# Kernel optimization log

Measured on AMD Instinct MI355X. Metric: run time of the kernel, lower is better.

The kernel has to match this reference:

```python
import jax, jax.numpy as jnp
import numpy as np
from math import sqrt

N_HEADS = 16

def setup_inputs() -> dict:
    key = jax.random.key(0)
    ks = jax.random.split(key, 6)
    B, T, C = 4, 2048, 1024
    s = 0.02
    return {
        "X": jax.random.normal(ks[0], (B, T, C), jnp.float32),
        "Wq": jax.random.normal(ks[1], (C, C), jnp.float32) * s,
        "Wk": jax.random.normal(ks[2], (C, C), jnp.float32) * s,
        "Wv": jax.random.normal(ks[3], (C, C), jnp.float32) * s,
        "Wo": jax.random.normal(ks[4], (C, C), jnp.float32) * s,
        "bo": jnp.zeros((C,), jnp.float32),
    }

def reference(X, Wq, Wk, Wv, Wo, bo):
    B, T, C = X.shape
    H = N_HEADS
    D = C // H
    scale = sqrt(C / H)  # == sqrt(D)
    # Linear layers (torch Linear: y = x @ W.T), split into heads: [B,H,T,D]
    Q = (X @ Wq.T).reshape(B, T, H, D).transpose(0, 2, 1, 3)
    K = (X @ Wk.T).reshape(B, T, H, D).transpose(0, 2, 1, 3)
    V = (X @ Wv.T).reshape(B, T, H, D).transpose(0, 2, 1, 3)
    A = jnp.einsum("bhtd,bhsd->bhts", Q, K) / scale  # [B,H,T,T]
    causal = jnp.tril(jnp.ones((T, T), dtype=bool))
    A = jnp.where(causal, A, -jnp.inf)
    A = jax.nn.softmax(A, axis=-1)
    Y = jnp.einsum("bhts,bhsd->bhtd", A, V)  # [B,H,T,D]
    Y = Y.transpose(0, 2, 1, 3).reshape(B, T, C)
    return Y @ Wo.T + bo
```

## Files before the change

### kernel.cpp

```cpp
#include <hip/hip_runtime.h>
#include <hip/hip_bf16.h>
#include <stdint.h>


typedef unsigned short u16;
typedef __attribute__((ext_vector_type(8))) __bf16 bf16x8;
typedef __attribute__((ext_vector_type(4))) float  f32x4;
typedef __attribute__((ext_vector_type(4))) unsigned short u16x4;
typedef __attribute__((ext_vector_type(8))) unsigned short u16x8;
typedef __attribute__((ext_vector_type(4))) short s16x4;

#define B_  4
#define T_  2048
#define C_  1024
#define H_  16
#define D_  64
#define BT_ (B_ * T_)
#define NT_ 16

#define Q_SCALE 0.1803368801111204f

__device__ __forceinline__ u16 f32_to_bf16(float f) {
    unsigned int u = __float_as_uint(f);
    unsigned int r = (u + 0x7FFFu + ((u >> 16) & 1u)) >> 16;
    return (u16)r;
}

__device__ __forceinline__ unsigned int pk_bf16(float a, float b) {
    float2 f2; f2.x = a; f2.y = b;
    __hip_bfloat162 h = __float22bfloat162_rn(f2);
    return *(unsigned int*)&h;
}

__device__ __forceinline__ void async16(const void* g, void* lds) {
    __builtin_amdgcn_global_load_lds(
        (const __attribute__((address_space(1))) void*)g,
        (__attribute__((address_space(3))) void*)lds, 16, 0, 0);
}

__global__ void cast_all_kernel(const float* __restrict__ X,
                                const float* __restrict__ w0, const float* __restrict__ w1,
                                const float* __restrict__ w2, const float* __restrict__ w3,
                                u16* __restrict__ xo,
                                u16* __restrict__ o0, u16* __restrict__ o1,
                                u16* __restrict__ o2, u16* __restrict__ o3) {
    int id = blockIdx.x;
    const float* in; u16* out; int i;
    if (id < 8192) {
        in = X; out = xo; i = id * 256 + threadIdx.x;
    } else {
        int k = (id - 8192) >> 10;
        in  = (k == 0) ? w0 : (k == 1) ? w1 : (k == 2) ? w2 : w3;
        out = (k == 0) ? o0 : (k == 1) ? o1 : (k == 2) ? o2 : o3;
        i = ((id - 8192) & 1023) * 256 + threadIdx.x;
    }
    float4 v = ((const float4*)in)[i];
    u16x4 o;
    o[0] = f32_to_bf16(v.x); o[1] = f32_to_bf16(v.y);
    o[2] = f32_to_bf16(v.z); o[3] = f32_to_bf16(v.w);
    ((u16x4*)out)[i] = o;
}

template<bool SWAP>
__device__ __forceinline__ void gemm8_core(const u16* __restrict__ Arow,
                                           const u16* __restrict__ Brow,
                                           char* lds, f32x4 (&acc)[4][4])
{
    int tid  = threadIdx.x;
    int lane = tid & 63, w = tid >> 6;
    int quad = lane >> 4, l15 = lane & 15;
    int wm = w >> 2, wn = w & 3;

    int r  = tid >> 2, s4 = tid & 3;
    int kg = ((s4 - (r >> 1)) & 3) * 8;
    const u16* xsrc  = Arow + (size_t)r * C_ + kg;
    const u16* wsrc0 = Brow + (size_t)r * C_ + kg;
    const u16* wsrc1 = Brow + (size_t)(128 + r) * C_ + kg;
    int wu = w << 10;

    int xoff[4], woff[4];
#pragma unroll
    for (int i = 0; i < 4; ++i) {
        int rx = wm * 64 + i * 16 + l15;
        xoff[i] = rx * 64 + (((rx >> 1) + quad) & 3) * 16;
        int rw = wn * 64 + i * 16 + l15;
        woff[i] = 16384 + rw * 64 + (((rw >> 1) + quad) & 3) * 16;
    }

    auto issue_group = [&](int g) {
        int db = (g >> 1) & 1, ks = g & 1;
        int koff = (g >> 1) * 64 + ks * 32;
        char* ldb = lds + db * 49152;
        async16(xsrc  + koff, ldb + ks * 8192 + wu);
        async16(wsrc0 + koff, ldb + 16384 + ks * 16384 + wu);
        async16(wsrc1 + koff, ldb + 16384 + ks * 16384 + 8192 + wu);
    };

    issue_group(0); issue_group(1); issue_group(2);
    asm volatile("s_waitcnt vmcnt(6)" ::: "memory");
    __builtin_amdgcn_s_barrier();
    asm volatile("" ::: "memory");

    for (int t = 0; t < NT_; ++t) {
        char* cb = lds + (t & 1) * 49152;
#pragma unroll
        for (int p = 0; p < 2; ++p) {
            bf16x8 xf[4], wf[4];
            const char* xb = cb + p * 8192;
            const char* wb = cb + p * 16384;
#pragma unroll
            for (int i = 0; i < 4; ++i) xf[i] = *(const bf16x8*)(xb + xoff[i]);
#pragma unroll
            for (int j = 0; j < 4; ++j) wf[j] = *(const bf16x8*)(wb + woff[j]);

            int g = 2 * t + 3 + p;
            if (g < 2 * NT_) issue_group(g);

            if (t < NT_ - 2) {
                asm volatile("s_waitcnt vmcnt(6)" ::: "memory");
            } else if (t == NT_ - 2) {
                if (p == 0) asm volatile("s_waitcnt vmcnt(6)" ::: "memory");
                else        asm volatile("s_waitcnt vmcnt(3)" ::: "memory");
            } else {
                if (p == 0) asm volatile("s_waitcnt vmcnt(0)" ::: "memory");
            }
            asm volatile("" ::: "memory");
            __builtin_amdgcn_s_barrier();
            asm volatile("" ::: "memory");

            __builtin_amdgcn_s_setprio(1);
#pragma unroll
            for (int i = 0; i < 4; ++i)
#pragma unroll
                for (int j = 0; j < 4; ++j) {
                    if (SWAP)
                        acc[i][j] = __builtin_amdgcn_mfma_f32_16x16x32_bf16(xf[i], wf[j], acc[i][j], 0, 0, 0);
                    else
                        acc[i][j] = __builtin_amdgcn_mfma_f32_16x16x32_bf16(wf[j], xf[i], acc[i][j], 0, 0, 0);
                }
            __builtin_amdgcn_s_setprio(0);
            asm volatile("" ::: "memory");
            __builtin_amdgcn_s_barrier();
            asm volatile("" ::: "memory");
        }
    }
}

__global__ __launch_bounds__(512, 2) void qkv_gemm8(
    const u16* __restrict__ Xb,
    const u16* __restrict__ Wqb, const u16* __restrict__ Wkb, const u16* __restrict__ Wvb,
    u16* __restrict__ Qb, u16* __restrict__ Kb, u16* __restrict__ Vtb)
{
    __shared__ __attribute__((aligned(128))) char LDSRAW[98304];

    int id = blockIdx.x;
    int wg = (id & 7) * 96 + (id >> 3);
    int bm = wg / 12, bn = wg % 12;
    int m0 = bm * 128;
    int nmat = bn >> 2;
    int chb  = (bn & 3) * 256;

    const u16* Wsel = (nmat == 0) ? Wqb : (nmat == 1) ? Wkb : Wvb;
    const u16* Arow = Xb   + (size_t)m0  * C_;
    const u16* Brow = Wsel + (size_t)chb * C_;

    f32x4 acc[4][4];
    const f32x4 z4 = {0.f, 0.f, 0.f, 0.f};
#pragma unroll
    for (int i = 0; i < 4; ++i)
#pragma unroll
        for (int j = 0; j < 4; ++j) acc[i][j] = z4;

    int tid = threadIdx.x, lane = tid & 63, w = tid >> 6;
    int quad = lane >> 4, l15 = lane & 15;
    int wm = w >> 2, wn = w & 3;

    if (nmat < 2) {
        gemm8_core<false>(Arow, Brow, LDSRAW, acc);
        u16* OUT = nmat ? Kb : Qb;
        float scale = nmat ? 1.0f : Q_SCALE;
#pragma unroll
        for (int i = 0; i < 4; ++i) {
            size_t trow = (size_t)(m0 + wm * 64 + i * 16 + l15) * C_;
#pragma unroll
            for (int j = 0; j < 4; ++j) {
                int ch = chb + wn * 64 + j * 16 + quad * 4;
                u16x4 v;
#pragma unroll
                for (int rr = 0; rr < 4; ++rr) v[rr] = f32_to_bf16(acc[i][j][rr] * scale);
                *(u16x4*)&OUT[trow + ch] = v;
            }
        }
    } else {
        gemm8_core<true>(Arow, Brow, LDSRAW, acc);
#pragma unroll
        for (int i = 0; i < 4; ++i) {
            int t0 = m0 + wm * 64 + i * 16 + quad * 4;
            int bb_ = t0 >> 11, tloc = t0 & (T_ - 1);
#pragma unroll
            for (int j = 0; j < 4; ++j) {
                int ch = chb + wn * 64 + j * 16 + l15;
                int h = ch >> 6, d = ch & 63;
                u16x4 v;
#pragma unroll
                for (int rr = 0; rr < 4; ++rr) v[rr] = f32_to_bf16(acc[i][j][rr]);
                *(u16x4*)&Vtb[(size_t)((bb_ * H_ + h) * D_ + d) * T_ + tloc] = v;
            }
        }
    }
}

__global__ __launch_bounds__(256, 4) void attn_kernel(
    const u16* __restrict__ Qb, const u16* __restrict__ Kb,
    const u16* __restrict__ Vtb, u16* __restrict__ Yb)
{
    __shared__ u16 SMA[16384];
    u16* Ks0 = SMA;
    u16* Ks1 = SMA + 4096;
    u16* Vs0 = SMA + 8192;
    u16* Vs1 = SMA + 12288;

    int id = blockIdx.x;
    int bh = id & 63;
    int jj = id >> 6;

    int tid = threadIdx.x, lane = tid & 63, w = tid >> 6;
    int quad = lane >> 4, l15 = lane & 15;
    int b = bh >> 4, h = bh & 15;

    int koff0[4], koff1[4], voff[4][4];
#pragma unroll
    for (int sblk = 0; sblk < 4; ++sblk) {
        int sr = sblk * 16 + l15;
        koff0[sblk] = (sr * 64 + ((quad + sr) & 7) * 8) * 2;
        koff1[sblk] = (sr * 64 + ((4 + quad + sr) & 7) * 8) * 2;
    }
#pragma unroll
    for (int n = 0; n < 4; ++n)
#pragma unroll
        for (int sblk = 0; sblk < 4; ++sblk) {
            int dr = n * 16 + l15;
            voff[n][sblk] = (dr * 64 + ((sblk * 2 + (quad >> 1) + dr) & 7) * 8 + (quad & 1) * 4) * 2;
        }

    int cA = tid, cB = tid + 256;
    int sA = cA >> 3, sB = cB >> 3;
    int offA = (((cA & 7) - sA) & 7) * 8;
    int offB = (((cB & 7) - sB) & 7) * 8;
    const u16* Kbase = Kb + (size_t)(b * T_) * C_ + h * 64;
    const u16* Vbase = Vtb + (size_t)bh * D_ * T_;
    int ldsb0 = (w * 64) * 16, ldsb1 = (256 + w * 64) * 16;

    const s16x4 ones = { (short)0x3F80, (short)0x3F80, (short)0x3F80, (short)0x3F80 };
    const f32x4 z4 = {0.f, 0.f, 0.f, 0.f};

    int qts[2] = { jj, 31 - jj };

    for (int pass = 0; pass < 2; ++pass) {
        int qt = qts[pass];
        int qbase = qt * 64;

        if (pass) __syncthreads();

        bf16x8 qf0, qf1;
        {
            const u16* q0 = Qb + ((size_t)(b * T_ + qbase + w * 16 + l15)) * C_ + h * 64;
            qf0 = *(const bf16x8*)(q0 + quad * 8);
            qf1 = *(const bf16x8*)(q0 + 32 + quad * 8);
        }

        f32x4 o_acc[4];
        f32x4 l_acc = z4;
#pragma unroll
        for (int n = 0; n < 4; ++n) o_acc[n] = z4;

        const int nst = qt + 1;

        const u16* kgpA = Kbase + (size_t)sA * C_ + offA;
        const u16* kgpB = Kbase + (size_t)sB * C_ + offB;
        const u16* vgpA = Vbase + sA * T_ + offA;
        const u16* vgpB = Vbase + sB * T_ + offB;

        async16(kgpA, (char*)Ks0 + ldsb0);
        async16(kgpB, (char*)Ks0 + ldsb1);
        async16(vgpA, (char*)Vs0 + ldsb0);
        async16(vgpB, (char*)Vs0 + ldsb1);
        kgpA += 64 * C_; kgpB += 64 * C_; vgpA += 64; vgpB += 64;

        auto tile_body = [&](int st, const u16* K_, const u16* V_, char* Kpf, char* Vpf) {
            __syncthreads();
            if (st + 1 < nst) {
                async16(kgpA, Kpf + ldsb0);
                async16(kgpB, Kpf + ldsb1);
                async16(vgpA, Vpf + ldsb0);
                async16(vgpB, Vpf + ldsb1);
            }
            kgpA += 64 * C_; kgpB += 64 * C_; vgpA += 64; vgpB += 64;

            f32x4 sv[4];
#pragma unroll
            for (int sblk = 0; sblk < 4; ++sblk) {
                bf16x8 k0 = *(const bf16x8*)((const char*)K_ + koff0[sblk]);
                bf16x8 k1 = *(const bf16x8*)((const char*)K_ + koff1[sblk]);
                f32x4 t0 = __builtin_amdgcn_mfma_f32_16x16x32_bf16(k0, qf0, z4, 0, 0, 0);
                sv[sblk] = __builtin_amdgcn_mfma_f32_16x16x32_bf16(k1, qf1, t0, 0, 0, 0);
            }

            if (st == qt) {
                int tl = w * 16 + l15;
#pragma unroll
                for (int sblk = 0; sblk < 4; ++sblk)
#pragma unroll
                    for (int r = 0; r < 4; ++r)
                        if (sblk * 16 + quad * 4 + r > tl) sv[sblk][r] = -1e30f;
            }

            s16x4 pfrag[4];
#pragma unroll
            for (int sblk = 0; sblk < 4; ++sblk) {
#pragma unroll
                for (int r = 0; r < 4; ++r)
                    sv[sblk][r] = __builtin_amdgcn_exp2f(sv[sblk][r]);
                uint2 pk;
                pk.x = pk_bf16(sv[sblk][0], sv[sblk][1]);
                pk.y = pk_bf16(sv[sblk][2], sv[sblk][3]);
                pfrag[sblk] = *(s16x4*)&pk;
                l_acc = __builtin_amdgcn_mfma_f32_16x16x16bf16_1k(ones, pfrag[sblk], l_acc, 0, 0, 0);
            }

#pragma unroll
            for (int n = 0; n < 4; ++n)
#pragma unroll
                for (int sblk = 0; sblk < 4; ++sblk) {
                    s16x4 va = *(const s16x4*)((const char*)V_ + voff[n][sblk]);
                    o_acc[n] = __builtin_amdgcn_mfma_f32_16x16x16bf16_1k(va, pfrag[sblk], o_acc[n], 0, 0, 0);
                }
        };

        for (int st = 0; st < nst; st += 2) {
            tile_body(st, Ks0, Vs0, (char*)Ks1, (char*)Vs1);
            if (st + 1 < nst)
                tile_body(st + 1, Ks1, Vs1, (char*)Ks0, (char*)Vs0);
        }

        __syncthreads();
        u16* PW = SMA + w * 1152;
        {
            float inv = 1.0f / l_acc[0];
#pragma unroll
            for (int n = 0; n < 4; ++n) {
                uint2 pk;
                pk.x = pk_bf16(o_acc[n][0] * inv, o_acc[n][1] * inv);
                pk.y = pk_bf16(o_acc[n][2] * inv, o_acc[n][3] * inv);
                *(u16x4*)&PW[l15 * 72 + n * 16 + quad * 4] = *(u16x4*)&pk;
            }
        }
        asm volatile("s_waitcnt lgkmcnt(0)" ::: "memory");
#pragma unroll
        for (int st = 0; st < 2; ++st) {
            int tr = st * 8 + (lane >> 3);
            int d8 = (lane & 7) * 8;
            u16x8 v = *(u16x8*)&PW[tr * 72 + d8];
            *(u16x8*)&Yb[(size_t)(b * T_ + qbase + w * 16 + tr) * C_ + h * 64 + d8] = v;
        }
    }
}

__global__ __launch_bounds__(512, 2) void proj_gemm8(
    const u16* __restrict__ Yb, const u16* __restrict__ Wob,
    const float* __restrict__ bo, float* __restrict__ out)
{
    __shared__ __attribute__((aligned(128))) char LDSRAW[98304];

    int id = blockIdx.x;
    int wg = (id & 7) * 32 + (id >> 3);
    int bm = wg >> 2, bn = wg & 3;
    int m0 = bm * 128, n0 = bn * 256;

    f32x4 acc[4][4];
    const f32x4 z4 = {0.f, 0.f, 0.f, 0.f};
#pragma unroll
    for (int i = 0; i < 4; ++i)
#pragma unroll
        for (int j = 0; j < 4; ++j) acc[i][j] = z4;

    gemm8_core<false>(Yb + (size_t)m0 * C_, Wob + (size_t)n0 * C_, LDSRAW, acc);

    int tid = threadIdx.x, lane = tid & 63, w = tid >> 6;
    int quad = lane >> 4, l15 = lane & 15;
    int wm = w >> 2, wn = w & 3;

#pragma unroll
    for (int j = 0; j < 4; ++j) {
        int ch = n0 + wn * 64 + j * 16 + quad * 4;
        f32x4 bv = *(const f32x4*)&bo[ch];
#pragma unroll
        for (int i = 0; i < 4; ++i) {
            int t = m0 + wm * 64 + i * 16 + l15;
            f32x4 v = acc[i][j] + bv;
            *(f32x4*)&out[(size_t)t * C_ + ch] = v;
        }
    }
}

extern "C" void kernel_launch(void* const* d_in, const int* in_sizes, int n_in,
                              void* d_out, int out_size, void* d_ws, size_t ws_size,
                              hipStream_t stream) {
    const float* X  = (const float*)d_in[0];
    const float* Wq = (const float*)d_in[1];
    const float* Wk = (const float*)d_in[2];
    const float* Wv = (const float*)d_in[3];
    const float* Wo = (const float*)d_in[4];
    const float* bo = (const float*)d_in[5];

    char* ws = (char*)d_ws;
    u16* Xb  = (u16*)(ws);
    u16* Wqb = (u16*)(ws + (16u << 20));
    u16* Wkb = (u16*)(ws + (18u << 20));
    u16* Wvb = (u16*)(ws + (20u << 20));
    u16* Wob = (u16*)(ws + (22u << 20));
    u16* Qb  = (u16*)(ws + (24u << 20));
    u16* Kb  = (u16*)(ws + (40u << 20));
    u16* Vtb = (u16*)(ws + (56u << 20));
    u16* Yb  = (u16*)(ws + (72u << 20));

    cast_all_kernel<<<dim3(8192 + 4 * 1024), 256, 0, stream>>>(
        X, Wq, Wk, Wv, Wo, Xb, Wqb, Wkb, Wvb, Wob);

    qkv_gemm8<<<dim3(768), 512, 0, stream>>>(Xb, Wqb, Wkb, Wvb, Qb, Kb, Vtb);
    attn_kernel<<<dim3(1024), 256, 0, stream>>>(Qb, Kb, Vtb, Yb);
    proj_gemm8<<<dim3(256), 512, 0, stream>>>(Yb, Wob, bo, (float*)d_out);
}
```

Before: 242.2 us.

## Replace QKV GEMM with 256x256 tiles and quarter-phase pipelined loads

Replaces the 128x256-tile QKV projection GEMM with a 256x256-tile kernel using 128 KB of double-buffered LDS and a four-phase schedule. Each phase interleaves async global loads for the next K-tile with MFMA work on one quadrant of the tile, gated by fine-grained vmcnt waits. This halves the grid to 384 blocks and raises arithmetic intensity per loaded byte. The cost is more accumulator registers per thread (32 f32x4) and more LDS per block, so occupancy drops, and fewer blocks may leave some CUs with uneven work on 256 CUs.

```diff
diff --git a/kernel.cpp b/kernel.cpp
--- a/kernel.cpp
+++ b/kernel.cpp
@@ -61,6 +61,183 @@
     ((u16x4*)out)[i] = o;
 }
 
+#define QPHASE(CB, MH, NH, DOISSUE, G, GATE)                                      \
+  {                                                                               \
+    if ((NH) == 0) {                                                              \
+      _Pragma("unroll")                                                           \
+      for (int f = 0; f < 4; ++f) {                                               \
+        _Pragma("unroll")                                                         \
+        for (int ks = 0; ks < 2; ++ks)                                            \
+          xf[f][ks] = *(const bf16x8*)((CB) + (MH) * 16384 + axoff[f][ks]);       \
+      }                                                                           \
+    }                                                                             \
+    if ((MH) == 0) {                                                              \
+      _Pragma("unroll")                                                           \
+      for (int e = 0; e < 2; ++e) {                                               \
+        _Pragma("unroll")                                                         \
+        for (int ks = 0; ks < 2; ++ks)                                            \
+          wf[NH][e][ks] = *(const bf16x8*)((CB) + (NH) * 16384 + bwoff[e][ks]);   \
+      }                                                                           \
+    }                                                                             \
+    if (DOISSUE) issue_unit(G);                                                   \
+    if ((GATE) == 4)      asm volatile("s_waitcnt vmcnt(4)" ::: "memory");        \
+    else if ((GATE) == 2) asm volatile("s_waitcnt vmcnt(2)" ::: "memory");        \
+    else if ((GATE) == 0) asm volatile("s_waitcnt vmcnt(0)" ::: "memory");        \
+    __builtin_amdgcn_s_barrier();                                                 \
+    asm volatile("" ::: "memory");                                                \
+    __builtin_amdgcn_s_setprio(1);                                                \
+    _Pragma("unroll")                                                             \
+    for (int f = 0; f < 4; ++f) {                                                 \
+      _Pragma("unroll")                                                           \
+      for (int e = 0; e < 2; ++e) {                                               \
+        f32x4 a_ = acc[(MH) * 4 + f][(NH) * 2 + e];                               \
+        if (SWAPV) {                                                              \
+          a_ = __builtin_amdgcn_mfma_f32_16x16x32_bf16(xf[f][0], wf[NH][e][0], a_, 0, 0, 0); \
+          a_ = __builtin_amdgcn_mfma_f32_16x16x32_bf16(xf[f][1], wf[NH][e][1], a_, 0, 0, 0); \
+        } else {                                                                  \
+          a_ = __builtin_amdgcn_mfma_f32_16x16x32_bf16(wf[NH][e][0], xf[f][0], a_, 0, 0, 0); \
+          a_ = __builtin_amdgcn_mfma_f32_16x16x32_bf16(wf[NH][e][1], xf[f][1], a_, 0, 0, 0); \
+        }                                                                         \
+        acc[(MH) * 4 + f][(NH) * 2 + e] = a_;                                     \
+      }                                                                           \
+    }                                                                             \
+    __builtin_amdgcn_s_setprio(0);                                                \
+    asm volatile("" ::: "memory");                                                \
+    __builtin_amdgcn_s_barrier();                                                 \
+    asm volatile("" ::: "memory");                                                \
+  }
+
+template<bool SWAPV>
+__device__ __forceinline__ void qkv256_core(const u16* __restrict__ Arow,
+                                            const u16* __restrict__ Brow,
+                                            char* lds, f32x4 (&acc)[8][4])
+{
+    int tid  = threadIdx.x;
+    int lane = tid & 63, w = tid >> 6;
+    int quad = lane >> 4, l15 = lane & 15;
+    int wm = w >> 2, wn = w & 3;
+
+    int gc = (((tid & 7) - (tid >> 3)) & 7) * 8;
+    const u16* xsrc0 = Arow + (size_t)(tid >> 3) * C_ + gc;
+    const u16* xsrc1 = xsrc0 + (size_t)64 * C_;
+    const u16* wsrc0 = Brow + (size_t)(tid >> 3) * C_ + gc;
+    const u16* wsrc1 = wsrc0 + (size_t)64 * C_;
+
+    auto issue_unit = [&](int g) {
+        int u = g & 3, kt = g >> 2;
+        char* d = lds + ((kt & 1) << 16) + (u << 14) + (w << 10);
+        size_t off = (size_t)(u & 1) * (128 * C_) + (size_t)kt * 64;
+        const u16* s0 = (u < 2) ? xsrc0 : wsrc0;
+        const u16* s1 = (u < 2) ? xsrc1 : wsrc1;
+        async16(s0 + off, d);
+        async16(s1 + off, d + 8192);
+    };
+
+    int axoff[4][2], bwoff[2][2];
+#pragma unroll
+    for (int f = 0; f < 4; ++f) {
+        int r = wm * 64 + f * 16 + l15;
+#pragma unroll
+        for (int ks = 0; ks < 2; ++ks)
+            axoff[f][ks] = r * 128 + (((ks * 4 + quad + r) & 7) << 4);
+    }
+#pragma unroll
+    for (int e = 0; e < 2; ++e) {
+        int r = wn * 32 + e * 16 + l15;
+#pragma unroll
+        for (int ks = 0; ks < 2; ++ks)
+            bwoff[e][ks] = 32768 + r * 128 + (((ks * 4 + quad + r) & 7) << 4);
+    }
+
+    bf16x8 xf[4][2];
+    bf16x8 wf[2][2][2];
+
+    issue_unit(0); issue_unit(2); issue_unit(3); issue_unit(1);
+    asm volatile("s_waitcnt vmcnt(4)" ::: "memory");
+    __builtin_amdgcn_s_barrier();
+    asm volatile("" ::: "memory");
+
+    for (int t = 0; t < NT_ - 1; ++t) {
+        char* cb = lds + ((t & 1) << 16);
+        int g4 = (t + 1) << 2;
+        QPHASE(cb, 0, 0, 1, g4 + 0, 4);
+        QPHASE(cb, 0, 1, 1, g4 + 2, 4);
+        QPHASE(cb, 1, 0, 1, g4 + 3, -1);
+        QPHASE(cb, 1, 1, 1, g4 + 1, 4);
+    }
+    {
+        char* cb = lds + (((NT_ - 1) & 1) << 16);
+        QPHASE(cb, 0, 0, 0, 0, 2);
+        QPHASE(cb, 0, 1, 0, 0, 0);
+        QPHASE(cb, 1, 0, 0, 0, -1);
+        QPHASE(cb, 1, 1, 0, 0, -1);
+    }
+}
+
+__global__ __launch_bounds__(512, 2) void qkv_gemm256(
+    const u16* __restrict__ Xb,
+    const u16* __restrict__ Wqb, const u16* __restrict__ Wkb, const u16* __restrict__ Wvb,
+    u16* __restrict__ Qb, u16* __restrict__ Kb, u16* __restrict__ Vtb)
+{
+    __shared__ __attribute__((aligned(128))) char LDSRAW[131072];
+
+    int id = blockIdx.x;
+    int wg = (id & 7) * 48 + (id >> 3);
+    int bm = wg / 12, bn = wg % 12;
+    int m0 = bm * 256;
+    int nmat = bn >> 2;
+    int chb  = (bn & 3) * 256;
+
+    const u16* Wsel = (nmat == 0) ? Wqb : (nmat == 1) ? Wkb : Wvb;
+    const u16* Arow = Xb   + (size_t)m0  * C_;
+    const u16* Brow = Wsel + (size_t)chb * C_;
+
+    f32x4 acc[8][4];
+    const f32x4 z4 = {0.f, 0.f, 0.f, 0.f};
+#pragma unroll
+    for (int i = 0; i < 8; ++i)
+#pragma unroll
+        for (int j = 0; j < 4; ++j) acc[i][j] = z4;
+
+    int tid = threadIdx.x, lane = tid & 63, w = tid >> 6;
+    int quad = lane >> 4, l15 = lane & 15;
+    int wm = w >> 2, wn = w & 3;
+
+    if (nmat < 2) {
+        qkv256_core<false>(Arow, Brow, LDSRAW, acc);
+        u16* OUT = nmat ? Kb : Qb;
+        float scale = nmat ? 1.0f : Q_SCALE;
+#pragma unroll
+        for (int mi = 0; mi < 8; ++mi) {
+            size_t trow = (size_t)(m0 + (mi >> 2) * 128 + wm * 64 + (mi & 3) * 16 + l15) * C_;
+#pragma unroll
+            for (int nj = 0; nj < 4; ++nj) {
+                int ch = chb + (nj >> 1) * 128 + wn * 32 + (nj & 1) * 16 + quad * 4;
+                u16x4 v;
+#pragma unroll
+                for (int rr = 0; rr < 4; ++rr) v[rr] = f32_to_bf16(acc[mi][nj][rr] * scale);
+                *(u16x4*)&OUT[trow + ch] = v;
+            }
+        }
+    } else {
+        qkv256_core<true>(Arow, Brow, LDSRAW, acc);
+#pragma unroll
+        for (int mi = 0; mi < 8; ++mi) {
+            int t0 = m0 + (mi >> 2) * 128 + wm * 64 + (mi & 3) * 16 + quad * 4;
+            int bb_ = t0 >> 11, tloc = t0 & (T_ - 1);
+#pragma unroll
+            for (int nj = 0; nj < 4; ++nj) {
+                int ch = chb + (nj >> 1) * 128 + wn * 32 + (nj & 1) * 16 + l15;
+                int h = ch >> 6, d = ch & 63;
+                u16x4 v;
+#pragma unroll
+                for (int rr = 0; rr < 4; ++rr) v[rr] = f32_to_bf16(acc[mi][nj][rr]);
+                *(u16x4*)&Vtb[(size_t)((bb_ * H_ + h) * D_ + d) * T_ + tloc] = v;
+            }
+        }
+    }
+}
+
 template<bool SWAP>
 __device__ __forceinline__ void gemm8_core(const u16* __restrict__ Arow,
                                            const u16* __restrict__ Brow,
@@ -146,70 +323,6 @@
     }
 }
 
-__global__ __launch_bounds__(512, 2) void qkv_gemm8(
-    const u16* __restrict__ Xb,
-    const u16* __restrict__ Wqb, const u16* __restrict__ Wkb, const u16* __restrict__ Wvb,
-    u16* __restrict__ Qb, u16* __restrict__ Kb, u16* __restrict__ Vtb)
-{
-    __shared__ __attribute__((aligned(128))) char LDSRAW[98304];
-
-    int id = blockIdx.x;
-    int wg = (id & 7) * 96 + (id >> 3);
-    int bm = wg / 12, bn = wg % 12;
-    int m0 = bm * 128;
-    int nmat = bn >> 2;
-    int chb  = (bn & 3) * 256;
-
-    const u16* Wsel = (nmat == 0) ? Wqb : (nmat == 1) ? Wkb : Wvb;
-    const u16* Arow = Xb   + (size_t)m0  * C_;
-    const u16* Brow = Wsel + (size_t)chb * C_;
-
-    f32x4 acc[4][4];
-    const f32x4 z4 = {0.f, 0.f, 0.f, 0.f};
-#pragma unroll
-    for (int i = 0; i < 4; ++i)
-#pragma unroll
-        for (int j = 0; j < 4; ++j) acc[i][j] = z4;
-
-    int tid = threadIdx.x, lane = tid & 63, w = tid >> 6;
-    int quad = lane >> 4, l15 = lane & 15;
-    int wm = w >> 2, wn = w & 3;
-
-    if (nmat < 2) {
-        gemm8_core<false>(Arow, Brow, LDSRAW, acc);
-        u16* OUT = nmat ? Kb : Qb;
-        float scale = nmat ? 1.0f : Q_SCALE;
-#pragma unroll
-        for (int i = 0; i < 4; ++i) {
-            size_t trow = (size_t)(m0 + wm * 64 + i * 16 + l15) * C_;
-#pragma unroll
-            for (int j = 0; j < 4; ++j) {
-                int ch = chb + wn * 64 + j * 16 + quad * 4;
-                u16x4 v;
-#pragma unroll
-                for (int rr = 0; rr < 4; ++rr) v[rr] = f32_to_bf16(acc[i][j][rr] * scale);
-                *(u16x4*)&OUT[trow + ch] = v;
-            }
-        }
-    } else {
-        gemm8_core<true>(Arow, Brow, LDSRAW, acc);
-#pragma unroll
-        for (int i = 0; i < 4; ++i) {
-            int t0 = m0 + wm * 64 + i * 16 + quad * 4;
-            int bb_ = t0 >> 11, tloc = t0 & (T_ - 1);
-#pragma unroll
-            for (int j = 0; j < 4; ++j) {
-                int ch = chb + wn * 64 + j * 16 + l15;
-                int h = ch >> 6, d = ch & 63;
-                u16x4 v;
-#pragma unroll
-                for (int rr = 0; rr < 4; ++rr) v[rr] = f32_to_bf16(acc[i][j][rr]);
-                *(u16x4*)&Vtb[(size_t)((bb_ * H_ + h) * D_ + d) * T_ + tloc] = v;
-            }
-        }
-    }
-}
-
 __global__ __launch_bounds__(256, 4) void attn_kernel(
     const u16* __restrict__ Qb, const u16* __restrict__ Kb,
     const u16* __restrict__ Vtb, u16* __restrict__ Yb)
@@ -427,7 +540,7 @@
     cast_all_kernel<<<dim3(8192 + 4 * 1024), 256, 0, stream>>>(
         X, Wq, Wk, Wv, Wo, Xb, Wqb, Wkb, Wvb, Wob);
 
-    qkv_gemm8<<<dim3(768), 512, 0, stream>>>(Xb, Wqb, Wkb, Wvb, Qb, Kb, Vtb);
+    qkv_gemm256<<<dim3(384), 512, 0, stream>>>(Xb, Wqb, Wkb, Wvb, Qb, Kb, Vtb);
     attn_kernel<<<dim3(1024), 256, 0, stream>>>(Qb, Kb, Vtb, Yb);
     proj_gemm8<<<dim3(256), 512, 0, stream>>>(Yb, Wob, bo, (float*)d_out);
 }
```

After: 241.2 us. Within noise of the previous version (-0.4%).

## Replace QKV GEMM with 128x384 tiles over concatenated weights and phased pipeline

Applied to the files above, without the earlier changes.

The QKV projection moves from 128x256 tiles (768 blocks) to 128x384 tiles (512 blocks). Wq, Wk and Wv are treated as one contiguous 3072-row weight matrix, so a single tile can straddle the Q/K/V boundary. Each K step is split into three phases that interleave async global loads with MFMA work, using explicit vmcnt/lgkmcnt waits and 128 KB of LDS double buffering. The goal is more reuse of the X tile per load and better overlap of loads with compute. The cost is higher register and LDS pressure, plus scalar scattered V^T stores in the tile that straddles K and V. The code relies on the Wq/Wk/Wv buffers sitting contiguously in the workspace, which they do at offsets 16, 18 and 20 MB.

```diff
diff --git a/kernel.cpp b/kernel.cpp
--- a/kernel.cpp
+++ b/kernel.cpp
@@ -61,6 +61,170 @@
     ((u16x4*)out)[i] = o;
 }
 
+#define PH384(CB, P, ISSUE, GATE)                                              \
+  {                                                                            \
+    if ((P) == 0) {                                                            \
+      _Pragma("unroll") for (int mi = 0; mi < 4; ++mi)                         \
+        _Pragma("unroll") for (int ks = 0; ks < 2; ++ks)                       \
+          xf[mi][ks] = *(const bf16x8*)((CB) + axoff[mi][ks]);                 \
+    }                                                                          \
+    _Pragma("unroll") for (int e = 0; e < 2; ++e)                              \
+      _Pragma("unroll") for (int ks = 0; ks < 2; ++ks)                         \
+        wf[e][ks] = *(const bf16x8*)((CB) + bwoff[2 * (P) + e][ks]);           \
+    ISSUE;                                                                     \
+    if ((P) == 0) asm volatile("s_waitcnt lgkmcnt(8)" ::: "memory");           \
+    if ((GATE) == 6) asm volatile("s_waitcnt vmcnt(6)" ::: "memory");          \
+    else if ((GATE) == 0) asm volatile("s_waitcnt vmcnt(0)" ::: "memory");     \
+    __builtin_amdgcn_s_barrier();                                              \
+    asm volatile("" ::: "memory");                                             \
+    __builtin_amdgcn_s_setprio(1);                                             \
+    _Pragma("unroll") for (int mi = 0; mi < 4; ++mi)                           \
+      _Pragma("unroll") for (int e = 0; e < 2; ++e) {                          \
+        f32x4 a_ = acc[mi][2 * (P) + e];                                       \
+        if (SWAPV) {                                                           \
+          a_ = __builtin_amdgcn_mfma_f32_16x16x32_bf16(xf[mi][0], wf[e][0], a_, 0, 0, 0); \
+          a_ = __builtin_amdgcn_mfma_f32_16x16x32_bf16(xf[mi][1], wf[e][1], a_, 0, 0, 0); \
+        } else {                                                               \
+          a_ = __builtin_amdgcn_mfma_f32_16x16x32_bf16(wf[e][0], xf[mi][0], a_, 0, 0, 0); \
+          a_ = __builtin_amdgcn_mfma_f32_16x16x32_bf16(wf[e][1], xf[mi][1], a_, 0, 0, 0); \
+        }                                                                      \
+        acc[mi][2 * (P) + e] = a_;                                             \
+      }                                                                        \
+    __builtin_amdgcn_s_setprio(0);                                             \
+    asm volatile("" ::: "memory");                                             \
+    __builtin_amdgcn_s_barrier();                                              \
+    asm volatile("" ::: "memory");                                             \
+  }
+
+template<bool SWAPV>
+__device__ __forceinline__ void qkv384_core(const u16* __restrict__ Arow,
+                                            const u16* __restrict__ Brow,
+                                            char* lds, f32x4 (&acc)[4][6])
+{
+    int tid = threadIdx.x, lane = tid & 63, w = tid >> 6;
+    int quad = lane >> 4, l15 = lane & 15;
+    int wm = w >> 2, wn = w & 3;
+
+    int gc = (((tid & 7) - (tid >> 3)) & 7) * 8;
+    const u16* asrc = Arow + (size_t)(tid >> 3) * C_ + gc;
+    const u16* bsrc = Brow + (size_t)(tid >> 3) * C_ + gc;
+
+    auto issue_unit = [&](int kt, int u) {
+        char* d = lds + ((kt & 1) << 16) + (u << 14) + (w << 10);
+        int ko = kt * 64;
+        const u16* s = (u == 0) ? (asrc + ko)
+                                : (bsrc + (size_t)(u - 1) * 128 * C_ + ko);
+        async16(s, d);
+        async16(s + (size_t)64 * C_, d + 8192);
+    };
+
+    int axoff[4][2], bwoff[6][2];
+#pragma unroll
+    for (int mi = 0; mi < 4; ++mi) {
+        int r = wm * 64 + mi * 16 + l15;
+#pragma unroll
+        for (int ks = 0; ks < 2; ++ks)
+            axoff[mi][ks] = r * 128 + (((ks * 4 + quad + r) & 7) << 4);
+    }
+#pragma unroll
+    for (int nj = 0; nj < 6; ++nj) {
+        int r = wn * 32 + (nj & 1) * 16 + l15;
+#pragma unroll
+        for (int ks = 0; ks < 2; ++ks)
+            bwoff[nj][ks] = (1 + (nj >> 1)) * 16384 + r * 128 + (((ks * 4 + quad + r) & 7) << 4);
+    }
+
+    bf16x8 xf[4][2];
+    bf16x8 wf[2][2];
+
+    issue_unit(0, 0); issue_unit(0, 1); issue_unit(0, 2); issue_unit(0, 3);
+    issue_unit(1, 0); issue_unit(1, 1); issue_unit(1, 2);
+    asm volatile("s_waitcnt vmcnt(6)" ::: "memory");
+    __builtin_amdgcn_s_barrier();
+    asm volatile("" ::: "memory");
+
+    for (int t = 0; t < NT_; ++t) {
+        char* cb = lds + ((t & 1) << 16);
+        PH384(cb, 0, { if (t + 1 < NT_) issue_unit(t + 1, 3); }, -1);
+        PH384(cb, 1, { if (t + 2 < NT_) { issue_unit(t + 2, 0); issue_unit(t + 2, 1); } }, -1);
+        int gate = (t < NT_ - 2) ? 6 : ((t == NT_ - 2) ? 0 : -1);
+        PH384(cb, 2, { if (t + 2 < NT_) issue_unit(t + 2, 2); }, gate);
+    }
+}
+
+__global__ __launch_bounds__(512, 2) void qkv_gemm384(
+    const u16* __restrict__ Xb, const u16* __restrict__ Wcat,
+    u16* __restrict__ Qb, u16* __restrict__ Kb, u16* __restrict__ Vtb)
+{
+    __shared__ __attribute__((aligned(128))) char LDSRAW[131072];
+
+    int id = blockIdx.x;
+    int wg = (id & 7) * 64 + (id >> 3);
+    int bn = wg >> 6;
+    int bm = wg & 63;
+    int m0 = bm * 128;
+    int chb = bn * 384;
+
+    const u16* Arow = Xb   + (size_t)m0  * C_;
+    const u16* Brow = Wcat + (size_t)chb * C_;
+
+    f32x4 acc[4][6];
+    const f32x4 z4 = {0.f, 0.f, 0.f, 0.f};
+#pragma unroll
+    for (int i = 0; i < 4; ++i)
+#pragma unroll
+        for (int j = 0; j < 6; ++j) acc[i][j] = z4;
+
+    int tid = threadIdx.x, lane = tid & 63, w = tid >> 6;
+    int quad = lane >> 4, l15 = lane & 15;
+    int wm = w >> 2, wn = w & 3;
+
+    if (bn < 6) {
+        qkv384_core<false>(Arow, Brow, LDSRAW, acc);
+#pragma unroll
+        for (int mi = 0; mi < 4; ++mi) {
+            int tg = m0 + wm * 64 + mi * 16 + l15;
+#pragma unroll
+            for (int nj = 0; nj < 6; ++nj) {
+                int colb = chb + (nj >> 1) * 128 + wn * 32 + (nj & 1) * 16 + quad * 4;
+                if (colb < 2048) {
+                    u16* OUT = (colb < 1024) ? Qb : Kb;
+                    float sc = (colb < 1024) ? Q_SCALE : 1.0f;
+                    u16x4 v;
+#pragma unroll
+                    for (int rr = 0; rr < 4; ++rr) v[rr] = f32_to_bf16(acc[mi][nj][rr] * sc);
+                    *(u16x4*)&OUT[(size_t)tg * C_ + (colb & 1023)] = v;
+                } else {
+                    int b_ = tg >> 11, tl = tg & (T_ - 1);
+#pragma unroll
+                    for (int rr = 0; rr < 4; ++rr) {
+                        int ch = colb + rr;
+                        int h = (ch >> 6) & 15, d = ch & 63;
+                        Vtb[((size_t)(b_ * H_ + h) * D_ + d) * T_ + tl] =
+                            f32_to_bf16(acc[mi][nj][rr]);
+                    }
+                }
+            }
+        }
+    } else {
+        qkv384_core<true>(Arow, Brow, LDSRAW, acc);
+#pragma unroll
+        for (int mi = 0; mi < 4; ++mi) {
+            int t0 = m0 + wm * 64 + mi * 16 + quad * 4;
+            int b_ = t0 >> 11, tl = t0 & (T_ - 1);
+#pragma unroll
+            for (int nj = 0; nj < 6; ++nj) {
+                int ch = chb + (nj >> 1) * 128 + wn * 32 + (nj & 1) * 16 + l15;
+                int h = (ch >> 6) & 15, d = ch & 63;
+                u16x4 v;
+#pragma unroll
+                for (int rr = 0; rr < 4; ++rr) v[rr] = f32_to_bf16(acc[mi][nj][rr]);
+                *(u16x4*)&Vtb[((size_t)(b_ * H_ + h) * D_ + d) * T_ + tl] = v;
+            }
+        }
+    }
+}
+
 template<bool SWAP>
 __device__ __forceinline__ void gemm8_core(const u16* __restrict__ Arow,
                                            const u16* __restrict__ Brow,
@@ -146,70 +310,6 @@
     }
 }
 
-__global__ __launch_bounds__(512, 2) void qkv_gemm8(
-    const u16* __restrict__ Xb,
-    const u16* __restrict__ Wqb, const u16* __restrict__ Wkb, const u16* __restrict__ Wvb,
-    u16* __restrict__ Qb, u16* __restrict__ Kb, u16* __restrict__ Vtb)
-{
-    __shared__ __attribute__((aligned(128))) char LDSRAW[98304];
-
-    int id = blockIdx.x;
-    int wg = (id & 7) * 96 + (id >> 3);
-    int bm = wg / 12, bn = wg % 12;
-    int m0 = bm * 128;
-    int nmat = bn >> 2;
-    int chb  = (bn & 3) * 256;
-
-    const u16* Wsel = (nmat == 0) ? Wqb : (nmat == 1) ? Wkb : Wvb;
-    const u16* Arow = Xb   + (size_t)m0  * C_;
-    const u16* Brow = Wsel + (size_t)chb * C_;
-
-    f32x4 acc[4][4];
-    const f32x4 z4 = {0.f, 0.f, 0.f, 0.f};
-#pragma unroll
-    for (int i = 0; i < 4; ++i)
-#pragma unroll
-        for (int j = 0; j < 4; ++j) acc[i][j] = z4;
-
-    int tid = threadIdx.x, lane = tid & 63, w = tid >> 6;
-    int quad = lane >> 4, l15 = lane & 15;
-    int wm = w >> 2, wn = w & 3;
-
-    if (nmat < 2) {
-        gemm8_core<false>(Arow, Brow, LDSRAW, acc);
-        u16* OUT = nmat ? Kb : Qb;
-        float scale = nmat ? 1.0f : Q_SCALE;
-#pragma unroll
-        for (int i = 0; i < 4; ++i) {
-            size_t trow = (size_t)(m0 + wm * 64 + i * 16 + l15) * C_;
-#pragma unroll
-            for (int j = 0; j < 4; ++j) {
-                int ch = chb + wn * 64 + j * 16 + quad * 4;
-                u16x4 v;
-#pragma unroll
-                for (int rr = 0; rr < 4; ++rr) v[rr] = f32_to_bf16(acc[i][j][rr] * scale);
-                *(u16x4*)&OUT[trow + ch] = v;
-            }
-        }
-    } else {
-        gemm8_core<true>(Arow, Brow, LDSRAW, acc);
-#pragma unroll
-        for (int i = 0; i < 4; ++i) {
-            int t0 = m0 + wm * 64 + i * 16 + quad * 4;
-            int bb_ = t0 >> 11, tloc = t0 & (T_ - 1);
-#pragma unroll
-            for (int j = 0; j < 4; ++j) {
-                int ch = chb + wn * 64 + j * 16 + l15;
-                int h = ch >> 6, d = ch & 63;
-                u16x4 v;
-#pragma unroll
-                for (int rr = 0; rr < 4; ++rr) v[rr] = f32_to_bf16(acc[i][j][rr]);
-                *(u16x4*)&Vtb[(size_t)((bb_ * H_ + h) * D_ + d) * T_ + tloc] = v;
-            }
-        }
-    }
-}
-
 __global__ __launch_bounds__(256, 4) void attn_kernel(
     const u16* __restrict__ Qb, const u16* __restrict__ Kb,
     const u16* __restrict__ Vtb, u16* __restrict__ Yb)
@@ -427,7 +527,7 @@
     cast_all_kernel<<<dim3(8192 + 4 * 1024), 256, 0, stream>>>(
         X, Wq, Wk, Wv, Wo, Xb, Wqb, Wkb, Wvb, Wob);
 
-    qkv_gemm8<<<dim3(768), 512, 0, stream>>>(Xb, Wqb, Wkb, Wvb, Qb, Kb, Vtb);
+    qkv_gemm384<<<dim3(512), 512, 0, stream>>>(Xb, Wqb, Qb, Kb, Vtb);
     attn_kernel<<<dim3(1024), 256, 0, stream>>>(Qb, Kb, Vtb, Yb);
     proj_gemm8<<<dim3(256), 512, 0, stream>>>(Yb, Wob, bo, (float*)d_out);
 }
```

Result: faster. 228.4 us (-5.7%).
